# Performance work log

Hardware: AMD Instinct MI355X
Metric: run time of the kernel (lower is better)

## Reference

```python
import jax, jax.numpy as jnp
import numpy as np
from jax import lax

H_PARAM = 10
DMAX = 3
L = 2 * H_PARAM * H_PARAM + 2 * H_PARAM + 1  # 221 chain length
HEIGHT = H_PARAM + 1   # 11
WIDTH = 2 * H_PARAM + 1  # 21
B, N = 256, 128
INIT_STD = 1e-9


def setup_inputs() -> dict:
    key = jax.random.key(0)
    k1, k2 = jax.random.split(key)
    samples = jax.random.normal(k1, (B, N, HEIGHT, WIDTH, DMAX), dtype=jnp.float32)
    tensors1 = INIT_STD * jax.random.normal(k2, (L, DMAX, DMAX, DMAX), dtype=jnp.float32)
    bias_mat = jnp.eye(DMAX, dtype=jnp.float32)[None, :, :]  # [1, D, D]
    return {"samples": samples, "tensors1": tensors1, "bias_mat": bias_mat}


def reference(samples, tensors1, bias_mat):
    b, n = samples.shape[0], samples.shape[1]
    D = tensors1.shape[-1]
    # [B*N, HW, D] then keep only the L positions actually contracted
    s = samples.reshape(b * n, -1, D)[:, : tensors1.shape[0], :]
    s_seq = jnp.moveaxis(s, 1, 0)  # [L, BN, D]
    eye_bias = bias_mat[0]         # [D, D]
    init = jnp.zeros((b * n, D), dtype=samples.dtype).at[:, 0].set(1.0)

    def step(vec, xs):
        x, T = xs  # x: [BN, D], T: [D, D, D]
        mats = jnp.einsum('bd,lrd->blr', x, T) + eye_bias  # [BN, D, D]
        vec = jnp.einsum('bl,blr->br', vec, mats)          # [BN, D]
        return vec, None

    vec, _ = lax.scan(step, init, (s_seq, tensors1))
    return vec.reshape(b, n, D)
```

## Files before the change

### kernel.cpp

```cpp
#include <hip/hip_runtime.h>

#define BN        32768
#define ESTRIDE   693
#define L_REAL    221
#define CHUNK     14
#define CDW       42
#define NGRP      4

__global__ __launch_bounds__(256, 6)
void mps_worker(const float* __restrict__ samples,
                const float* __restrict__ tensors,
                float* __restrict__ ws)
{
    __shared__ float lds_p[256 * 9];

    const int tid = threadIdx.x;
    const int eg  = blockIdx.x >> 2;
    const int cg  = blockIdx.x & 3;
    const int e0  = eg * 64;
    const int w   = tid >> 6;
    const int b   = tid & 63;
    const int ck  = __builtin_amdgcn_readfirstlane(cg * 4 + w);

    const float* xp = samples + (size_t)(e0 + b) * ESTRIDE + ck * CDW;
    float xq[CDW];
    #pragma unroll
    for (int j = 0; j < CDW; ++j) xq[j] = xp[j];

    float P[9] = {1.f, 0.f, 0.f, 0.f, 1.f, 0.f, 0.f, 0.f, 1.f};

    #pragma unroll
    for (int s = 0; s < CHUNK; ++s) {
        const int l = ck * CHUNK + s;
        if (l < L_REAL) {
            const float* Tg = tensors + l * 27;
            float Ts[27];
            #pragma unroll
            for (int j = 0; j < 27; ++j) Ts[j] = Tg[j];

            const float x0 = xq[s * 3 + 0];
            const float x1 = xq[s * 3 + 1];
            const float x2 = xq[s * 3 + 2];

            float E[9];
            #pragma unroll
            for (int l2 = 0; l2 < 3; ++l2)
                #pragma unroll
                for (int r = 0; r < 3; ++r)
                    E[l2 * 3 + r] = x0 * Ts[l2 * 9 + r * 3 + 0]
                                  + x1 * Ts[l2 * 9 + r * 3 + 1]
                                  + x2 * Ts[l2 * 9 + r * 3 + 2];

            #pragma unroll
            for (int i = 0; i < 3; ++i) {
                const float p0 = P[i * 3 + 0], p1 = P[i * 3 + 1], p2 = P[i * 3 + 2];
                P[i * 3 + 0] = p0 + (p0 * E[0] + p1 * E[3] + p2 * E[6]);
                P[i * 3 + 1] = p1 + (p0 * E[1] + p1 * E[4] + p2 * E[7]);
                P[i * 3 + 2] = p2 + (p0 * E[2] + p1 * E[5] + p2 * E[8]);
            }
        }
    }

    {
        float* pb = lds_p + tid * 9;
        #pragma unroll
        for (int k = 0; k < 9; ++k) pb[k] = P[k];
    }
    __syncthreads();

    if (tid < 64) {
        float G[9];
        #pragma unroll
        for (int k = 0; k < 9; ++k) G[k] = lds_p[tid * 9 + k];
        #pragma unroll
        for (int w2 = 1; w2 < 4; ++w2) {
            const float* q = lds_p + (w2 * 64 + tid) * 9;
            float N[9];
            #pragma unroll
            for (int i = 0; i < 3; ++i)
                #pragma unroll
                for (int r = 0; r < 3; ++r)
                    N[i * 3 + r] = G[i * 3 + 0] * q[0 + r]
                                 + G[i * 3 + 1] * q[3 + r]
                                 + G[i * 3 + 2] * q[6 + r];
            #pragma unroll
            for (int k = 0; k < 9; ++k) G[k] = N[k];
        }
        #pragma unroll
        for (int k = 0; k < 9; ++k)
            ws[((size_t)(cg * 9 + k) << 15) + (size_t)(e0 + tid)] = G[k];
    }
}

__global__ __launch_bounds__(256)
void mps_combine(const float* __restrict__ ws, float* __restrict__ out)
{
    const int e = blockIdx.x * 256 + threadIdx.x;
    float v0 = ws[(size_t)(0 << 15) + e];
    float v1 = ws[(size_t)(1 << 15) + e];
    float v2 = ws[(size_t)(2 << 15) + e];
    #pragma unroll
    for (int g = 1; g < NGRP; ++g) {
        float q[9];
        #pragma unroll
        for (int k = 0; k < 9; ++k)
            q[k] = ws[((size_t)(g * 9 + k) << 15) + e];
        float n0 = v0 * q[0] + v1 * q[3] + v2 * q[6];
        float n1 = v0 * q[1] + v1 * q[4] + v2 * q[7];
        float n2 = v0 * q[2] + v1 * q[5] + v2 * q[8];
        v0 = n0; v1 = n1; v2 = n2;
    }
    float* o = out + (size_t)e * 3;
    o[0] = v0; o[1] = v1; o[2] = v2;
}

extern "C" void kernel_launch(void* const* d_in, const int* in_sizes, int n_in,
                              void* d_out, int out_size, void* d_ws, size_t ws_size,
                              hipStream_t stream)
{
    const float* samples = (const float*)d_in[0];
    const float* tensors = (const float*)d_in[1];
    float* out = (float*)d_out;
    float* ws  = (float*)d_ws;
    (void)ws_size;

    mps_worker<<<dim3(512 * NGRP), dim3(256), 0, stream>>>(samples, tensors, ws);
    mps_combine<<<dim3(BN / 256), dim3(256), 0, stream>>>(ws, out);
}
```

Measured before the change: 30.50 us.

## Fuse combine into worker via last-block atomic counter and XCD-aware block mapping

Removes the separate combine kernel launch: each worker block bumps a per-element-group atomic counter, and the last of the four chunk-group blocks to finish multiplies the partial 3x3 products and writes the output. Block indices are also remapped so the four chunk groups of an element group land on the same XCD, which should keep the workspace traffic in that XCD's L2. This adds a hipMemsetAsync to clear the counters plus threadfences and atomics. The extra memset may cost about as much as the kernel launch it replaces.

```diff
diff --git a/kernel.cpp b/kernel.cpp
--- a/kernel.cpp
+++ b/kernel.cpp
@@ -6,17 +6,25 @@
 #define CHUNK     14
 #define CDW       42
 #define NGRP      4
+#define NEG       512
+#define WS_G_FLOATS (NGRP * 9 * BN)
 
 __global__ __launch_bounds__(256, 6)
 void mps_worker(const float* __restrict__ samples,
                 const float* __restrict__ tensors,
-                float* __restrict__ ws)
+                float* __restrict__ ws,
+                int* __restrict__ cnt,
+                float* __restrict__ out)
 {
     __shared__ float lds_p[256 * 9];
+    __shared__ int lds_old;
 
     const int tid = threadIdx.x;
-    const int eg  = blockIdx.x >> 2;
-    const int cg  = blockIdx.x & 3;
+    const int x   = blockIdx.x;
+    const int xcd = x & 7;
+    const int j   = x >> 3;
+    const int cg  = j & 3;
+    const int eg  = ((j >> 2) << 3) | xcd;
     const int e0  = eg * 64;
     const int w   = tid >> 6;
     const int b   = tid & 63;
@@ -25,7 +33,7 @@
     const float* xp = samples + (size_t)(e0 + b) * ESTRIDE + ck * CDW;
     float xq[CDW];
     #pragma unroll
-    for (int j = 0; j < CDW; ++j) xq[j] = xp[j];
+    for (int jj = 0; jj < CDW; ++jj) xq[jj] = xp[jj];
 
     float P[9] = {1.f, 0.f, 0.f, 0.f, 1.f, 0.f, 0.f, 0.f, 1.f};
 
@@ -36,7 +44,7 @@
             const float* Tg = tensors + l * 27;
             float Ts[27];
             #pragma unroll
-            for (int j = 0; j < 27; ++j) Ts[j] = Tg[j];
+            for (int jj = 0; jj < 27; ++jj) Ts[jj] = Tg[jj];
 
             const float x0 = xq[s * 3 + 0];
             const float x1 = xq[s * 3 + 1];
@@ -90,28 +98,34 @@
         for (int k = 0; k < 9; ++k)
             ws[((size_t)(cg * 9 + k) << 15) + (size_t)(e0 + tid)] = G[k];
     }
-}
 
-__global__ __launch_bounds__(256)
-void mps_combine(const float* __restrict__ ws, float* __restrict__ out)
-{
-    const int e = blockIdx.x * 256 + threadIdx.x;
-    float v0 = ws[(size_t)(0 << 15) + e];
-    float v1 = ws[(size_t)(1 << 15) + e];
-    float v2 = ws[(size_t)(2 << 15) + e];
-    #pragma unroll
-    for (int g = 1; g < NGRP; ++g) {
-        float q[9];
+    __syncthreads();
+    if (tid == 0) {
+        __threadfence();
+        lds_old = atomicAdd(&cnt[eg], 1);
+    }
+    __syncthreads();
+
+    if (lds_old == 3 && tid < 64) {
+        __threadfence();
+        const int e = e0 + tid;
+        float v0 = ws[(size_t)(0 << 15) + e];
+        float v1 = ws[(size_t)(1 << 15) + e];
+        float v2 = ws[(size_t)(2 << 15) + e];
         #pragma unroll
-        for (int k = 0; k < 9; ++k)
-            q[k] = ws[((size_t)(g * 9 + k) << 15) + e];
-        float n0 = v0 * q[0] + v1 * q[3] + v2 * q[6];
-        float n1 = v0 * q[1] + v1 * q[4] + v2 * q[7];
-        float n2 = v0 * q[2] + v1 * q[5] + v2 * q[8];
-        v0 = n0; v1 = n1; v2 = n2;
+        for (int g = 1; g < NGRP; ++g) {
+            float q[9];
+            #pragma unroll
+            for (int k = 0; k < 9; ++k)
+                q[k] = ws[((size_t)(g * 9 + k) << 15) + e];
+            float n0 = v0 * q[0] + v1 * q[3] + v2 * q[6];
+            float n1 = v0 * q[1] + v1 * q[4] + v2 * q[7];
+            float n2 = v0 * q[2] + v1 * q[5] + v2 * q[8];
+            v0 = n0; v1 = n1; v2 = n2;
+        }
+        float* o = out + (size_t)e * 3;
+        o[0] = v0; o[1] = v1; o[2] = v2;
     }
-    float* o = out + (size_t)e * 3;
-    o[0] = v0; o[1] = v1; o[2] = v2;
 }
 
 extern "C" void kernel_launch(void* const* d_in, const int* in_sizes, int n_in,
@@ -122,8 +136,11 @@
     const float* tensors = (const float*)d_in[1];
     float* out = (float*)d_out;
     float* ws  = (float*)d_ws;
+    int*   cnt = (int*)((char*)d_ws + (size_t)WS_G_FLOATS * sizeof(float));
     (void)ws_size;
 
-    mps_worker<<<dim3(512 * NGRP), dim3(256), 0, stream>>>(samples, tensors, ws);
-    mps_combine<<<dim3(BN / 256), dim3(256), 0, stream>>>(ws, out);
+    hipMemsetAsync(cnt, 0, NEG * sizeof(int), stream);
+
+    mps_worker<<<dim3(NEG * NGRP), dim3(256), 0, stream>>>(samples, tensors,
+                                                           ws, cnt, out);
 }
```

Measured after the change: 102.5 us. 3.36x slower.
